# Kernel optimization log

Measured on AMD Instinct MI355X. Metric: run time of the kernel, lower is better.

Reference implementation:

```python
import jax, jax.numpy as jnp
import numpy as np


def _masked_var(x, mask):
    # unbiased variance (torch.var default, ddof=1) over entries where mask==1
    cnt = jnp.sum(mask)
    mean = jnp.sum(x * mask) / jnp.maximum(cnt, 1.0)
    return jnp.sum(mask * (x - mean) ** 2) / jnp.maximum(cnt - 1.0, 1.0)


def setup_inputs() -> dict:
    key = jax.random.key(0)
    ks = jax.random.split(key, 9)
    B, N, F = 4, 8192, 64
    points = jax.random.normal(ks[0], (B, N, 3), dtype=jnp.float32)
    features = jax.random.normal(ks[1], (B, N, F), dtype=jnp.float32)
    leaf_mask = jax.random.randint(ks[2], (B, N), 0, 2).astype(bool)
    W1 = jax.random.normal(ks[3], (64, F + 3), dtype=jnp.float32) * 0.05
    b1 = jax.random.normal(ks[4], (64,), dtype=jnp.float32) * 0.05
    W2 = jax.random.normal(ks[5], (32, 64), dtype=jnp.float32) * 0.05
    b2 = jax.random.normal(ks[6], (32,), dtype=jnp.float32) * 0.05
    W3 = jax.random.normal(ks[7], (1, 32), dtype=jnp.float32) * 0.05
    b3 = jax.random.normal(ks[8], (1,), dtype=jnp.float32) * 0.05
    return {"points": points, "features": features, "leaf_mask": leaf_mask,
            "W1": W1, "b1": b1, "W2": W2, "b2": b2, "W3": W3, "b3": b3}


def reference(points, features, leaf_mask, W1, b1, W2, b2, W3, b3):
    # NOTE: in the original Torch code combined_feat = [feat(F), xyz(3), var(1)]
    # (length F+4) is truncated to expected_input_dim = F+3, so the kNN feature
    # variance is provably dropped. The MLP input is exactly [feat, xyz].
    B, N, _ = points.shape

    def mlp(x):  # x: [N, F+3]
        h = jax.nn.relu(x @ W1.T + b1)
        h = jax.nn.relu(h @ W2.T + b2)
        return jax.nn.sigmoid(h @ W3.T + b3)[:, 0]

    def per_batch(pts, feats, mask):
        maskf = mask.astype(pts.dtype)
        x = jnp.concatenate([feats, pts], axis=-1)  # [N, F+3]
        scores = mlp(x) * maskf  # non-leaf points stay 0
        n_leaf = jnp.sum(maskf)
        scores = jnp.where(n_leaf < 10.0, jnp.zeros_like(scores), scores)

        # separation confidence
        clarity = _masked_var(scores, maskf)
        sel = scores > 0.7
        cnt = jnp.sum(sel.astype(jnp.int32))
        idx = jnp.arange(N)
        order = jnp.argsort(jnp.where(sel, idx, N + idx))  # selected first, in order
        g = pts[order]  # [N,3]
        d = jnp.linalg.norm(g[1:] - g[:-1], axis=1)  # consecutive boundary-point dists
        pair_mask = (jnp.arange(N - 1) < cnt - 1).astype(pts.dtype)
        dvar = _masked_var(d, pair_mask)
        cont = jnp.clip(1.0 / (dvar + 1e-8), 0.0, 1.0)
        cont = jnp.where(cnt > 5, cont, 0.0)
        conf = jnp.clip(clarity * cont, 0.0, 1.0)
        conf = jnp.where(n_leaf == 0.0, 0.0, conf)
        return scores, conf

    boundary_prob, separation_confidence = jax.vmap(per_batch)(points, features, leaf_mask)
    return boundary_prob, features, separation_confidence
```

## Files before the change

kernel.cpp:

```cpp
#include <hip/hip_runtime.h>
#include <hip/hip_bf16.h>
#include <math.h>

#define NB 4
#define NPTS 8192
#define TOTAL_PTS (NB * NPTS)
#define OUT_FEAT_OFF 32768
#define OUT_CONF_OFF (32768 + 2097152)

__global__ __launch_bounds__(128) void mlp_kernel(
    const float* __restrict__ pts,
    const float* __restrict__ feats,
    const int* __restrict__ mask,
    const float* __restrict__ W1,
    const float* __restrict__ b1,
    const float* __restrict__ W2,
    const float* __restrict__ b2,
    const float* __restrict__ W3,
    const float* __restrict__ b3,
    float* __restrict__ out)
{
    __shared__ float sW1[67 * 64];
    __shared__ float sW2[64 * 32];
    __shared__ float sB1[64];
    __shared__ float sB2[32];
    __shared__ float sW3[32];
    __shared__ float sB3;

    const int t = threadIdx.x;
    const int p = blockIdx.x * 128 + t;

    for (int idx = t; idx < 67 * 64; idx += 128) {
        const int k = idx >> 6, j = idx & 63;
        sW1[idx] = W1[j * 67 + k];
    }
    for (int idx = t; idx < 64 * 32; idx += 128) {
        const int k = idx >> 5, j = idx & 31;
        sW2[idx] = W2[j * 64 + k];
    }
    if (t < 64) sB1[t] = b1[t];
    else if (t < 96) sB2[t - 64] = b2[t - 64];
    else sW3[t - 96] = W3[t - 96];
    if (t == 0) sB3 = b3[0];

    {
        const float4* fsrc = (const float4*)feats + (size_t)blockIdx.x * 2048;
        float4* fdst = (float4*)(out + OUT_FEAT_OFF) + (size_t)blockIdx.x * 2048;
#pragma unroll
        for (int i = 0; i < 16; ++i)
            fdst[i * 128 + t] = fsrc[i * 128 + t];
    }
    __syncthreads();

    float h1[64];
#pragma unroll
    for (int j = 0; j < 64; ++j) h1[j] = sB1[j];

    const float4* fx = (const float4*)feats + (size_t)p * 16;
    for (int kc = 0; kc < 16; ++kc) {
        const float4 xv = fx[kc];
        const float* r0 = &sW1[(4 * kc + 0) * 64];
        const float* r1 = &sW1[(4 * kc + 1) * 64];
        const float* r2 = &sW1[(4 * kc + 2) * 64];
        const float* r3 = &sW1[(4 * kc + 3) * 64];
#pragma unroll
        for (int j4 = 0; j4 < 16; ++j4) {
            const float4 a = *(const float4*)&r0[4 * j4];
            const float4 b = *(const float4*)&r1[4 * j4];
            const float4 c = *(const float4*)&r2[4 * j4];
            const float4 d = *(const float4*)&r3[4 * j4];
            h1[4*j4+0] = fmaf(xv.x,a.x, fmaf(xv.y,b.x, fmaf(xv.z,c.x, fmaf(xv.w,d.x, h1[4*j4+0]))));
            h1[4*j4+1] = fmaf(xv.x,a.y, fmaf(xv.y,b.y, fmaf(xv.z,c.y, fmaf(xv.w,d.y, h1[4*j4+1]))));
            h1[4*j4+2] = fmaf(xv.x,a.z, fmaf(xv.y,b.z, fmaf(xv.z,c.z, fmaf(xv.w,d.z, h1[4*j4+2]))));
            h1[4*j4+3] = fmaf(xv.x,a.w, fmaf(xv.y,b.w, fmaf(xv.z,c.w, fmaf(xv.w,d.w, h1[4*j4+3]))));
        }
    }
    const float px = pts[(size_t)p * 3 + 0];
    const float py = pts[(size_t)p * 3 + 1];
    const float pz = pts[(size_t)p * 3 + 2];
    {
        const float* r0 = &sW1[64 * 64];
        const float* r1 = &sW1[65 * 64];
        const float* r2 = &sW1[66 * 64];
#pragma unroll
        for (int j4 = 0; j4 < 16; ++j4) {
            const float4 a = *(const float4*)&r0[4 * j4];
            const float4 b = *(const float4*)&r1[4 * j4];
            const float4 c = *(const float4*)&r2[4 * j4];
            h1[4*j4+0] = fmaxf(fmaf(px,a.x, fmaf(py,b.x, fmaf(pz,c.x, h1[4*j4+0]))), 0.f);
            h1[4*j4+1] = fmaxf(fmaf(px,a.y, fmaf(py,b.y, fmaf(pz,c.y, h1[4*j4+1]))), 0.f);
            h1[4*j4+2] = fmaxf(fmaf(px,a.z, fmaf(py,b.z, fmaf(pz,c.z, h1[4*j4+2]))), 0.f);
            h1[4*j4+3] = fmaxf(fmaf(px,a.w, fmaf(py,b.w, fmaf(pz,c.w, h1[4*j4+3]))), 0.f);
        }
    }

    float h2[32];
#pragma unroll
    for (int j = 0; j < 32; ++j) h2[j] = sB2[j];
#pragma unroll
    for (int k = 0; k < 64; ++k) {
        const float hv = h1[k];
        const float* wr = &sW2[k * 32];
#pragma unroll
        for (int j4 = 0; j4 < 8; ++j4) {
            const float4 w = *(const float4*)&wr[4 * j4];
            h2[4*j4+0] = fmaf(hv, w.x, h2[4*j4+0]);
            h2[4*j4+1] = fmaf(hv, w.y, h2[4*j4+1]);
            h2[4*j4+2] = fmaf(hv, w.z, h2[4*j4+2]);
            h2[4*j4+3] = fmaf(hv, w.w, h2[4*j4+3]);
        }
    }

    float z = sB3;
#pragma unroll
    for (int j4 = 0; j4 < 8; ++j4) {
        const float4 w = *(const float4*)&sW3[4 * j4];
        z = fmaf(fmaxf(h2[4*j4+0], 0.f), w.x, z);
        z = fmaf(fmaxf(h2[4*j4+1], 0.f), w.y, z);
        z = fmaf(fmaxf(h2[4*j4+2], 0.f), w.z, z);
        z = fmaf(fmaxf(h2[4*j4+3], 0.f), w.w, z);
    }
    float s = 1.0f / (1.0f + expf(-z));
    if (mask[p] == 0) s = 0.0f;
    out[p] = s;
}

__device__ __forceinline__ float bsum(float v, volatile float* sred) {
#pragma unroll
    for (int o = 32; o; o >>= 1) v += __shfl_down(v, o, 64);
    const int w = threadIdx.x >> 6, l = threadIdx.x & 63;
    __syncthreads();
    if (l == 0) sred[w] = v;
    __syncthreads();
    if (threadIdx.x < 64) {
        float x = (l < 16) ? sred[l] : 0.f;
#pragma unroll
        for (int o = 8; o; o >>= 1) x += __shfl_down(x, o, 64);
        if (l == 0) sred[16] = x;
    }
    __syncthreads();
    return sred[16];
}

__device__ __forceinline__ int bscan_excl(int c, volatile int* sw, int* total) {
    const int w = threadIdx.x >> 6, l = threadIdx.x & 63;
    int incl = c;
#pragma unroll
    for (int o = 1; o < 64; o <<= 1) {
        const int n = __shfl_up(incl, o, 64);
        if (l >= o) incl += n;
    }
    __syncthreads();
    if (l == 63) sw[w] = incl;
    __syncthreads();
    if (threadIdx.x < 64) {
        const int v = (l < 16) ? sw[l] : 0;
        int iv = v;
#pragma unroll
        for (int o = 1; o < 16; o <<= 1) {
            const int n = __shfl_up(iv, o, 64);
            if (l >= o) iv += n;
        }
        if (l < 16) sw[l] = iv - v;
        if (l == 15) sw[16] = iv;
    }
    __syncthreads();
    *total = sw[16];
    return sw[w] + (incl - c);
}

__global__ __launch_bounds__(1024) void stats_kernel(
    const float* __restrict__ pts,
    const int* __restrict__ mask,
    float* __restrict__ out,
    float* __restrict__ ws)
{
    __shared__ float sred[32];
    __shared__ int sw[32];

    const int b = blockIdx.x;
    const int t = threadIdx.x;

    float* scores = out + (size_t)b * NPTS;
    const float* P = pts + (size_t)b * NPTS * 3;
    const int* M = mask + (size_t)b * NPTS;
    volatile float* g = (float*)ws + (size_t)b * 40960;
    volatile float* dd = (float*)ws + (size_t)b * 40960 + 3 * NPTS;

    const float4 sa = ((const float4*)scores)[2 * t];
    const float4 sb = ((const float4*)scores)[2 * t + 1];
    const int4 ma = ((const int4*)M)[2 * t];
    const int4 mb = ((const int4*)M)[2 * t + 1];
    float s[8] = {sa.x, sa.y, sa.z, sa.w, sb.x, sb.y, sb.z, sb.w};
    int mm[8] = {ma.x, ma.y, ma.z, ma.w, mb.x, mb.y, mb.z, mb.w};

    int cm = 0;
    float ss = 0.f;
#pragma unroll
    for (int i = 0; i < 8; ++i) {
        cm += (mm[i] != 0);
        ss += s[i];
    }
    const float nleaf = bsum((float)cm, sred);
    const float ssum = bsum(ss, sred);

    if (nleaf < 10.0f) {
        const float4 z4 = {0.f, 0.f, 0.f, 0.f};
        ((float4*)scores)[2 * t] = z4;
        ((float4*)scores)[2 * t + 1] = z4;
        if (t == 0) out[OUT_CONF_OFF + b] = 0.0f;
        return;
    }

    const float mean = ssum / fmaxf(nleaf, 1.0f);
    float vs = 0.f;
#pragma unroll
    for (int i = 0; i < 8; ++i) {
        if (mm[i] != 0) {
            const float d0 = s[i] - mean;
            vs += d0 * d0;
        }
    }
    const float clarity = bsum(vs, sred) / fmaxf(nleaf - 1.0f, 1.0f);

    int c0 = 0;
#pragma unroll
    for (int i = 0; i < 8; ++i) c0 += (s[i] > 0.7f);
    int cnt;
    int pos = bscan_excl(c0, sw, &cnt);
#pragma unroll
    for (int i = 0; i < 8; ++i) {
        if (s[i] > 0.7f) {
            const int idx = t * 8 + i;
            g[3 * pos + 0] = P[3 * idx + 0];
            g[3 * pos + 1] = P[3 * idx + 1];
            g[3 * pos + 2] = P[3 * idx + 2];
            ++pos;
        }
    }
    __syncthreads();

    const int npair = cnt - 1;
    float dsum = 0.f;
    for (int i = t; i < npair; i += 1024) {
        const float ax = g[3 * i + 0] - g[3 * i + 3];
        const float ay = g[3 * i + 1] - g[3 * i + 4];
        const float az = g[3 * i + 2] - g[3 * i + 5];
        const float d0 = sqrtf(ax * ax + ay * ay + az * az);
        dd[i] = d0;
        dsum += d0;
    }
    const float dtot = bsum(dsum, sred);
    const float npf = (float)npair;
    const float dmean = dtot / fmaxf(npf, 1.0f);
    float dv = 0.f;
    for (int i = t; i < npair; i += 1024) {
        const float e = dd[i] - dmean;
        dv += e * e;
    }
    const float dvar = bsum(dv, sred) / fmaxf(npf - 1.0f, 1.0f);

    float cont = fminf(fmaxf(1.0f / (dvar + 1e-8f), 0.0f), 1.0f);
    if (!(cnt > 5)) cont = 0.0f;
    const float conf = fminf(fmaxf(clarity * cont, 0.0f), 1.0f);
    if (t == 0) out[OUT_CONF_OFF + b] = conf;
}

extern "C" void kernel_launch(void* const* d_in, const int* in_sizes, int n_in,
                              void* d_out, int out_size, void* d_ws, size_t ws_size,
                              hipStream_t stream) {
    const float* points   = (const float*)d_in[0];
    const float* features = (const float*)d_in[1];
    const int*   leafmask = (const int*)d_in[2];
    const float* W1 = (const float*)d_in[3];
    const float* b1 = (const float*)d_in[4];
    const float* W2 = (const float*)d_in[5];
    const float* b2 = (const float*)d_in[6];
    const float* W3 = (const float*)d_in[7];
    const float* b3 = (const float*)d_in[8];
    float* out = (float*)d_out;
    float* ws = (float*)d_ws;

    mlp_kernel<<<TOTAL_PTS / 128, 128, 0, stream>>>(
        points, features, leafmask, W1, b1, W2, b2, W3, b3, out);
    stats_kernel<<<NB, 1024, 0, stream>>>(points, leafmask, out, ws);
}
```

Before: 108.7 us.

## Fuse MLP and stats kernels with last-block atomic counter, split hidden units

Merges the MLP kernel and the per-batch statistics kernel into one launch: each block bumps a per-batch atomic counter, and the last block of a batch computes variance, compaction and distance stats with 256 threads. The MLP now uses 256 threads per 128 points, two lanes per point, each computing half of layer 1 and a partial layer 2 combined by a cross-lane shuffle. This removes the second kernel launch and the serial gap between kernels, and halves per-thread registers for occupancy. In exchange it adds a memset, atomics and fences, and a stats tail run by fewer threads that each handle 32 elements.

```diff
diff --git a/kernel.cpp b/kernel.cpp
--- a/kernel.cpp
+++ b/kernel.cpp
@@ -8,7 +8,18 @@
 #define OUT_FEAT_OFF 32768
 #define OUT_CONF_OFF (32768 + 2097152)
 
-__global__ __launch_bounds__(128) void mlp_kernel(
+__device__ __forceinline__ float blockReduceSum256(float v) {
+    __shared__ float sred[4];
+#pragma unroll
+    for (int o = 32; o > 0; o >>= 1) v += __shfl_down(v, o, 64);
+    const int w = threadIdx.x >> 6, l = threadIdx.x & 63;
+    __syncthreads();
+    if (l == 0) sred[w] = v;
+    __syncthreads();
+    return sred[0] + sred[1] + sred[2] + sred[3];
+}
+
+__global__ __launch_bounds__(256) void fused_kernel(
     const float* __restrict__ pts,
     const float* __restrict__ feats,
     const int* __restrict__ mask,
@@ -18,7 +29,9 @@
     const float* __restrict__ b2,
     const float* __restrict__ W3,
     const float* __restrict__ b3,
-    float* __restrict__ out)
+    float* __restrict__ out,
+    int* __restrict__ counters,
+    float* __restrict__ wsf)
 {
     __shared__ float sW1[67 * 64];
     __shared__ float sW2[64 * 32];
@@ -26,45 +39,53 @@
     __shared__ float sB2[32];
     __shared__ float sW3[32];
     __shared__ float sB3;
+    __shared__ int sflag;
+    __shared__ int cnts[256];
 
     const int t = threadIdx.x;
-    const int p = blockIdx.x * 128 + t;
-
-    for (int idx = t; idx < 67 * 64; idx += 128) {
+
+    for (int idx = t; idx < 67 * 64; idx += 256) {
         const int k = idx >> 6, j = idx & 63;
         sW1[idx] = W1[j * 67 + k];
     }
-    for (int idx = t; idx < 64 * 32; idx += 128) {
+    for (int idx = t; idx < 64 * 32; idx += 256) {
         const int k = idx >> 5, j = idx & 31;
         sW2[idx] = W2[j * 64 + k];
     }
     if (t < 64) sB1[t] = b1[t];
     else if (t < 96) sB2[t - 64] = b2[t - 64];
-    else sW3[t - 96] = W3[t - 96];
+    else if (t < 128) sW3[t - 96] = W3[t - 96];
     if (t == 0) sB3 = b3[0];
 
     {
         const float4* fsrc = (const float4*)feats + (size_t)blockIdx.x * 2048;
         float4* fdst = (float4*)(out + OUT_FEAT_OFF) + (size_t)blockIdx.x * 2048;
 #pragma unroll
-        for (int i = 0; i < 16; ++i)
-            fdst[i * 128 + t] = fsrc[i * 128 + t];
-    }
-    __syncthreads();
-
-    float h1[64];
-#pragma unroll
-    for (int j = 0; j < 64; ++j) h1[j] = sB1[j];
+        for (int i = 0; i < 8; ++i)
+            fdst[i * 256 + t] = fsrc[i * 256 + t];
+    }
+    __syncthreads();
+
+    const int wv = t >> 6;
+    const int ln = t & 63;
+    const int half = ln >> 5;
+    const int pi = wv * 32 + (ln & 31);
+    const int p = blockIdx.x * 128 + pi;
+    const int joff = half * 32;
+
+    float h1[32];
+#pragma unroll
+    for (int j = 0; j < 32; ++j) h1[j] = sB1[joff + j];
 
     const float4* fx = (const float4*)feats + (size_t)p * 16;
     for (int kc = 0; kc < 16; ++kc) {
         const float4 xv = fx[kc];
-        const float* r0 = &sW1[(4 * kc + 0) * 64];
-        const float* r1 = &sW1[(4 * kc + 1) * 64];
-        const float* r2 = &sW1[(4 * kc + 2) * 64];
-        const float* r3 = &sW1[(4 * kc + 3) * 64];
-#pragma unroll
-        for (int j4 = 0; j4 < 16; ++j4) {
+        const float* r0 = &sW1[(4 * kc + 0) * 64 + joff];
+        const float* r1 = &sW1[(4 * kc + 1) * 64 + joff];
+        const float* r2 = &sW1[(4 * kc + 2) * 64 + joff];
+        const float* r3 = &sW1[(4 * kc + 3) * 64 + joff];
+#pragma unroll
+        for (int j4 = 0; j4 < 8; ++j4) {
             const float4 a = *(const float4*)&r0[4 * j4];
             const float4 b = *(const float4*)&r1[4 * j4];
             const float4 c = *(const float4*)&r2[4 * j4];
@@ -79,11 +100,11 @@
     const float py = pts[(size_t)p * 3 + 1];
     const float pz = pts[(size_t)p * 3 + 2];
     {
-        const float* r0 = &sW1[64 * 64];
-        const float* r1 = &sW1[65 * 64];
-        const float* r2 = &sW1[66 * 64];
-#pragma unroll
-        for (int j4 = 0; j4 < 16; ++j4) {
+        const float* r0 = &sW1[64 * 64 + joff];
+        const float* r1 = &sW1[65 * 64 + joff];
+        const float* r2 = &sW1[66 * 64 + joff];
+#pragma unroll
+        for (int j4 = 0; j4 < 8; ++j4) {
             const float4 a = *(const float4*)&r0[4 * j4];
             const float4 b = *(const float4*)&r1[4 * j4];
             const float4 c = *(const float4*)&r2[4 * j4];
@@ -96,11 +117,11 @@
 
     float h2[32];
 #pragma unroll
-    for (int j = 0; j < 32; ++j) h2[j] = sB2[j];
-#pragma unroll
-    for (int k = 0; k < 64; ++k) {
+    for (int j = 0; j < 32; ++j) h2[j] = half ? 0.0f : sB2[j];
+#pragma unroll
+    for (int k = 0; k < 32; ++k) {
         const float hv = h1[k];
-        const float* wr = &sW2[k * 32];
+        const float* wr = &sW2[(joff + k) * 32];
 #pragma unroll
         for (int j4 = 0; j4 < 8; ++j4) {
             const float4 w = *(const float4*)&wr[4 * j4];
@@ -110,6 +131,8 @@
             h2[4*j4+3] = fmaf(hv, w.w, h2[4*j4+3]);
         }
     }
+#pragma unroll
+    for (int j = 0; j < 32; ++j) h2[j] += __shfl_xor(h2[j], 32, 64);
 
     float z = sB3;
 #pragma unroll
@@ -120,118 +143,84 @@
         z = fmaf(fmaxf(h2[4*j4+2], 0.f), w.z, z);
         z = fmaf(fmaxf(h2[4*j4+3], 0.f), w.w, z);
     }
-    float s = 1.0f / (1.0f + expf(-z));
-    if (mask[p] == 0) s = 0.0f;
-    out[p] = s;
-}
-
-__device__ __forceinline__ float bsum(float v, volatile float* sred) {
-#pragma unroll
-    for (int o = 32; o; o >>= 1) v += __shfl_down(v, o, 64);
-    const int w = threadIdx.x >> 6, l = threadIdx.x & 63;
-    __syncthreads();
-    if (l == 0) sred[w] = v;
-    __syncthreads();
-    if (threadIdx.x < 64) {
-        float x = (l < 16) ? sred[l] : 0.f;
-#pragma unroll
-        for (int o = 8; o; o >>= 1) x += __shfl_down(x, o, 64);
-        if (l == 0) sred[16] = x;
-    }
-    __syncthreads();
-    return sred[16];
-}
-
-__device__ __forceinline__ int bscan_excl(int c, volatile int* sw, int* total) {
-    const int w = threadIdx.x >> 6, l = threadIdx.x & 63;
-    int incl = c;
-#pragma unroll
-    for (int o = 1; o < 64; o <<= 1) {
-        const int n = __shfl_up(incl, o, 64);
-        if (l >= o) incl += n;
-    }
-    __syncthreads();
-    if (l == 63) sw[w] = incl;
-    __syncthreads();
-    if (threadIdx.x < 64) {
-        const int v = (l < 16) ? sw[l] : 0;
-        int iv = v;
-#pragma unroll
-        for (int o = 1; o < 16; o <<= 1) {
-            const int n = __shfl_up(iv, o, 64);
-            if (l >= o) iv += n;
-        }
-        if (l < 16) sw[l] = iv - v;
-        if (l == 15) sw[16] = iv;
-    }
-    __syncthreads();
-    *total = sw[16];
-    return sw[w] + (incl - c);
-}
-
-__global__ __launch_bounds__(1024) void stats_kernel(
-    const float* __restrict__ pts,
-    const int* __restrict__ mask,
-    float* __restrict__ out,
-    float* __restrict__ ws)
-{
-    __shared__ float sred[32];
-    __shared__ int sw[32];
-
-    const int b = blockIdx.x;
-    const int t = threadIdx.x;
-
-    float* scores = out + (size_t)b * NPTS;
-    const float* P = pts + (size_t)b * NPTS * 3;
-    const int* M = mask + (size_t)b * NPTS;
-    volatile float* g = (float*)ws + (size_t)b * 40960;
-    volatile float* dd = (float*)ws + (size_t)b * 40960 + 3 * NPTS;
-
-    const float4 sa = ((const float4*)scores)[2 * t];
-    const float4 sb = ((const float4*)scores)[2 * t + 1];
-    const int4 ma = ((const int4*)M)[2 * t];
-    const int4 mb = ((const int4*)M)[2 * t + 1];
-    float s[8] = {sa.x, sa.y, sa.z, sa.w, sb.x, sb.y, sb.z, sb.w};
-    int mm[8] = {ma.x, ma.y, ma.z, ma.w, mb.x, mb.y, mb.z, mb.w};
-
-    int cm = 0;
+    float sc = 1.0f / (1.0f + expf(-z));
+    if (mask[p] == 0) sc = 0.0f;
+    if (half == 0) out[p] = sc;
+
+    const int batch = blockIdx.x >> 6;
+    __syncthreads();
+    if (t == 0) {
+        const int old = __hip_atomic_fetch_add(&counters[batch], 1,
+                                               __ATOMIC_ACQ_REL,
+                                               __HIP_MEMORY_SCOPE_AGENT);
+        sflag = (old == 63);
+    }
+    __syncthreads();
+    if (!sflag) return;
+    __builtin_amdgcn_fence(__ATOMIC_ACQUIRE, "agent");
+
+    float* scores = out + (size_t)batch * NPTS;
+    const float* P = pts + (size_t)batch * NPTS * 3;
+    const int* M = mask + (size_t)batch * NPTS;
+    float* g = wsf + (size_t)batch * 40960;
+    float* dd = g + 3 * NPTS;
+
+    float s[32];
+    unsigned int mbits = 0;
+#pragma unroll
+    for (int i = 0; i < 8; ++i) {
+        const float4 s4 = ((const float4*)scores)[t * 8 + i];
+        s[4*i+0] = s4.x; s[4*i+1] = s4.y; s[4*i+2] = s4.z; s[4*i+3] = s4.w;
+        const int4 m4 = ((const int4*)M)[t * 8 + i];
+        mbits |= (m4.x != 0 ? 1u : 0u) << (4*i+0);
+        mbits |= (m4.y != 0 ? 1u : 0u) << (4*i+1);
+        mbits |= (m4.z != 0 ? 1u : 0u) << (4*i+2);
+        mbits |= (m4.w != 0 ? 1u : 0u) << (4*i+3);
+    }
+
     float ss = 0.f;
 #pragma unroll
-    for (int i = 0; i < 8; ++i) {
-        cm += (mm[i] != 0);
-        ss += s[i];
-    }
-    const float nleaf = bsum((float)cm, sred);
-    const float ssum = bsum(ss, sred);
+    for (int i = 0; i < 32; ++i) ss += s[i];
+    const float nleaf = blockReduceSum256((float)__popc(mbits));
+    const float ssum = blockReduceSum256(ss);
 
     if (nleaf < 10.0f) {
         const float4 z4 = {0.f, 0.f, 0.f, 0.f};
-        ((float4*)scores)[2 * t] = z4;
-        ((float4*)scores)[2 * t + 1] = z4;
-        if (t == 0) out[OUT_CONF_OFF + b] = 0.0f;
+#pragma unroll
+        for (int i = 0; i < 8; ++i) ((float4*)scores)[t * 8 + i] = z4;
+        if (t == 0) out[OUT_CONF_OFF + batch] = 0.0f;
         return;
     }
 
     const float mean = ssum / fmaxf(nleaf, 1.0f);
     float vs = 0.f;
 #pragma unroll
-    for (int i = 0; i < 8; ++i) {
-        if (mm[i] != 0) {
+    for (int i = 0; i < 32; ++i) {
+        if (mbits & (1u << i)) {
             const float d0 = s[i] - mean;
             vs += d0 * d0;
         }
     }
-    const float clarity = bsum(vs, sred) / fmaxf(nleaf - 1.0f, 1.0f);
+    const float clarity = blockReduceSum256(vs) / fmaxf(nleaf - 1.0f, 1.0f);
 
     int c0 = 0;
 #pragma unroll
-    for (int i = 0; i < 8; ++i) c0 += (s[i] > 0.7f);
-    int cnt;
-    int pos = bscan_excl(c0, sw, &cnt);
-#pragma unroll
-    for (int i = 0; i < 8; ++i) {
+    for (int i = 0; i < 32; ++i) c0 += (s[i] > 0.7f);
+    cnts[t] = c0;
+    __syncthreads();
+    for (int off = 1; off < 256; off <<= 1) {
+        const int v = cnts[t];
+        const int a = (t >= off) ? cnts[t - off] : 0;
+        __syncthreads();
+        cnts[t] = v + a;
+        __syncthreads();
+    }
+    const int cnt = cnts[255];
+    int pos = cnts[t] - c0;
+#pragma unroll
+    for (int i = 0; i < 32; ++i) {
         if (s[i] > 0.7f) {
-            const int idx = t * 8 + i;
+            const int idx = t * 32 + i;
             g[3 * pos + 0] = P[3 * idx + 0];
             g[3 * pos + 1] = P[3 * idx + 1];
             g[3 * pos + 2] = P[3 * idx + 2];
@@ -242,7 +231,7 @@
 
     const int npair = cnt - 1;
     float dsum = 0.f;
-    for (int i = t; i < npair; i += 1024) {
+    for (int i = t; i < npair; i += 256) {
         const float ax = g[3 * i + 0] - g[3 * i + 3];
         const float ay = g[3 * i + 1] - g[3 * i + 4];
         const float az = g[3 * i + 2] - g[3 * i + 5];
@@ -250,20 +239,20 @@
         dd[i] = d0;
         dsum += d0;
     }
-    const float dtot = bsum(dsum, sred);
+    const float dtot = blockReduceSum256(dsum);
     const float npf = (float)npair;
     const float dmean = dtot / fmaxf(npf, 1.0f);
     float dv = 0.f;
-    for (int i = t; i < npair; i += 1024) {
+    for (int i = t; i < npair; i += 256) {
         const float e = dd[i] - dmean;
         dv += e * e;
     }
-    const float dvar = bsum(dv, sred) / fmaxf(npf - 1.0f, 1.0f);
+    const float dvar = blockReduceSum256(dv) / fmaxf(npf - 1.0f, 1.0f);
 
     float cont = fminf(fmaxf(1.0f / (dvar + 1e-8f), 0.0f), 1.0f);
     if (!(cnt > 5)) cont = 0.0f;
     const float conf = fminf(fmaxf(clarity * cont, 0.0f), 1.0f);
-    if (t == 0) out[OUT_CONF_OFF + b] = conf;
+    if (t == 0) out[OUT_CONF_OFF + batch] = conf;
 }
 
 extern "C" void kernel_launch(void* const* d_in, const int* in_sizes, int n_in,
@@ -279,9 +268,10 @@
     const float* W3 = (const float*)d_in[7];
     const float* b3 = (const float*)d_in[8];
     float* out = (float*)d_out;
-    float* ws = (float*)d_ws;
-
-    mlp_kernel<<<TOTAL_PTS / 128, 128, 0, stream>>>(
-        points, features, leafmask, W1, b1, W2, b2, W3, b3, out);
-    stats_kernel<<<NB, 1024, 0, stream>>>(points, leafmask, out, ws);
+    int* counters = (int*)d_ws;
+    float* wsf = (float*)d_ws + 64;
+
+    (void)hipMemsetAsync(d_ws, 0, 64, stream);
+    fused_kernel<<<256, 256, 0, stream>>>(
+        points, features, leafmask, W1, b1, W2, b2, W3, b3, out, counters, wsf);
 }
```

New measurement: 107.1 us. About the same (-1.5%).
